# Optimization experiments

Measured on AMD Instinct MI355X. Metric: run time of the kernel, lower is better.

## Reference

```python
import jax, jax.numpy as jnp
import numpy as np

N, E, F, H, C = 100000, 1600000, 128, 128, 16
NEG_SLOPE = 0.01  # torch F.leaky_relu default


def setup_inputs() -> dict:
    key = jax.random.key(0)
    ks = jax.random.split(key, 32)
    inp = {
        "x": jax.random.normal(ks[0], (N, F), jnp.float32),
        "edge_index": jax.random.randint(ks[1], (2, E), 0, N, jnp.int32),
        "edge_weight": jax.random.uniform(ks[2], (E,), jnp.float32),
    }
    def w(k, fan_in, fan_out):
        s = 1.0 / np.sqrt(fan_in)
        return jax.random.uniform(k, (fan_in, fan_out), jnp.float32, -s, s)
    # cell 0: pre 128->128, arma 128->128, sage 128->128
    inp["pre_w0"] = w(ks[3], F, H); inp["pre_b0"] = jnp.zeros((H,), jnp.float32)
    inp["arma_w0"] = w(ks[4], H, H); inp["arma_v0"] = w(ks[5], H, H); inp["arma_b0"] = jnp.zeros((H,), jnp.float32)
    inp["sage_wl0"] = w(ks[6], H, H); inp["sage_bl0"] = jnp.zeros((H,), jnp.float32); inp["sage_wr0"] = w(ks[7], H, H)
    # cell 1: pre 256->128 (cell0 outputs 2H)
    inp["pre_w1"] = w(ks[8], 2 * H, H); inp["pre_b1"] = jnp.zeros((H,), jnp.float32)
    inp["arma_w1"] = w(ks[9], H, H); inp["arma_v1"] = w(ks[10], H, H); inp["arma_b1"] = jnp.zeros((H,), jnp.float32)
    inp["sage_wl1"] = w(ks[11], H, H); inp["sage_bl1"] = jnp.zeros((H,), jnp.float32); inp["sage_wr1"] = w(ks[12], H, H)
    inp["cls_w"] = w(ks[13], 2 * H, C); inp["cls_b"] = jnp.zeros((C,), jnp.float32)
    return inp


def _cell(h, row, col, norm, ew, cnt, n, arma_w, arma_v, arma_b, sage_wl, sage_bl, sage_wr):
    # ARMAConv (num_stacks=1, num_layers=1): relu(A_hat (h W) + h V + b), A_hat = sym-norm adj (no self loops)
    t = h @ arma_w
    agg = jax.ops.segment_sum(norm[:, None] * t[row], col, num_segments=n)
    h1 = jax.nn.leaky_relu(jax.nn.relu(agg + h @ arma_v + arma_b), NEG_SLOPE)
    # SAGEConv (mean aggr of edge-weighted messages): lin_l(mean_j w_ij h_j) + lin_r(h_i)
    s = jax.ops.segment_sum(ew[:, None] * h[row], col, num_segments=n)
    h2 = jax.nn.leaky_relu((s / cnt[:, None]) @ sage_wl + sage_bl + h @ sage_wr, NEG_SLOPE)
    return jax.nn.elu(jnp.concatenate([h1, h2], axis=1))


def reference(x, edge_index, edge_weight,
              pre_w0, pre_b0, arma_w0, arma_v0, arma_b0, sage_wl0, sage_bl0, sage_wr0,
              pre_w1, pre_b1, arma_w1, arma_v1, arma_b1, sage_wl1, sage_bl1, sage_wr1,
              cls_w, cls_b):
    n = x.shape[0]
    row, col = edge_index[0], edge_index[1]  # messages flow row -> col
    # gcn_norm without self loops (ARMAConv)
    deg = jax.ops.segment_sum(edge_weight, col, num_segments=n)
    dinv = jnp.where(deg > 0, 1.0 / jnp.sqrt(jnp.where(deg > 0, deg, 1.0)), 0.0)
    norm = dinv[row] * edge_weight * dinv[col]
    # scatter_mean denominator (edge counts, clamped to 1)
    cnt = jnp.maximum(jax.ops.segment_sum(jnp.ones_like(edge_weight), col, num_segments=n), 1.0)
    h = x  # eval mode: input dropout is identity
    for p in [(pre_w0, pre_b0, arma_w0, arma_v0, arma_b0, sage_wl0, sage_bl0, sage_wr0),
              (pre_w1, pre_b1, arma_w1, arma_v1, arma_b1, sage_wl1, sage_bl1, sage_wr1)]:
        pw, pb = p[0], p[1]
        h = _cell(h @ pw + pb, row, col, norm, edge_weight, cnt, n, *p[2:])
    logits = h @ cls_w + cls_b
    return jax.nn.log_softmax(logits, axis=-1)
```

## Files before the change

### kernel.cpp

```cpp
#include <hip/hip_runtime.h>
#include <hip/hip_bf16.h>
#include <hip/hip_fp16.h>

typedef __bf16 bf16x8 __attribute__((ext_vector_type(8)));
typedef float f32x4 __attribute__((ext_vector_type(4)));
typedef unsigned short ushort_t;
typedef unsigned int uint_t;

#if defined(__has_builtin)
#if __has_builtin(__builtin_amdgcn_global_load_lds)
#define HAS_GLL 1
#endif
#endif

__device__ inline float blo(uint_t v) { return __uint_as_float(v << 16); }
__device__ inline float bhi(uint_t v) { return __uint_as_float(v & 0xffff0000u); }
__device__ inline ushort_t f2b(float f) {
  uint_t u = __float_as_uint(f);
  uint_t r = (u + 0x7fffu + ((u >> 16) & 1u)) >> 16;
  return (ushort_t)r;
}
__device__ inline uint_t pk2(float a, float b) {
  return (uint_t)f2b(a) | ((uint_t)f2b(b) << 16);
}


__global__ __launch_bounds__(256) void bcount_k(const int* __restrict__ col,
                                                int* __restrict__ bcnt, int E, int NB) {
  __shared__ int h[256];
  int t = threadIdx.x;
  h[t] = 0;
  __syncthreads();
  int e0 = blockIdx.x * 8192;
#pragma unroll
  for (int j = 0; j < 32; ++j) {
    int e = e0 + j * 256 + t;
    if (e < E) atomicAdd(&h[col[e] >> 9], 1);
  }
  __syncthreads();
  if (t < NB && h[t] > 0) atomicAdd(&bcnt[t], h[t]);
}

__global__ __launch_bounds__(256) void bscan_k(const int* __restrict__ bcnt,
                                               int* __restrict__ bbase, int* __restrict__ cursor,
                                               int* __restrict__ offs, int NB, int N, int E) {
  __shared__ int sd[256];
  int t = threadIdx.x;
  int v = (t < NB) ? bcnt[t] : 0;
  int acc = v;
  sd[t] = v; __syncthreads();
  for (int off = 1; off < 256; off <<= 1) {
    int x = (t >= off) ? sd[t - off] : 0;
    __syncthreads();
    acc += x; sd[t] = acc;
    __syncthreads();
  }
  if (t < NB) { bbase[t] = acc - v; cursor[t] = acc - v; }
  if (t == 0) { bbase[NB] = E; offs[N] = E; }
}

__global__ __launch_bounds__(512) void bscatter_k(
    const int* __restrict__ row, const int* __restrict__ col, const float* __restrict__ ew,
    int* __restrict__ cursor, uint2* __restrict__ eout, int E, int NB) {
  __shared__ int h[256];
  __shared__ int lofs[256];
  __shared__ int lcur[256];
  __shared__ int gbase[256];
  __shared__ int sc[256];
  __shared__ uint2 stage[8192];
  __shared__ int addr[8192];
  int t = threadIdx.x;
  int e0 = blockIdx.x * 8192;
  int cnt = min(8192, E - e0);
  if (t < 256) h[t] = 0;
  __syncthreads();
#pragma unroll
  for (int j = 0; j < 16; ++j) {
    int e = e0 + j * 512 + t;
    if (e < E) atomicAdd(&h[col[e] >> 9], 1);
  }
  __syncthreads();
  int s = (t < 256) ? h[t] : 0;
  int acc = s;
  if (t < 256) sc[t] = s;
  __syncthreads();
  for (int off = 1; off < 256; off <<= 1) {
    int x = (t < 256 && t >= off) ? sc[t - off] : 0;
    __syncthreads();
    if (t < 256) { acc += x; sc[t] = acc; }
    __syncthreads();
  }
  if (t < NB && s > 0) gbase[t] = atomicAdd(&cursor[t], s);
  if (t < 256) { lofs[t] = acc - s; lcur[t] = acc - s; }
  __syncthreads();
#pragma unroll
  for (int j = 0; j < 16; ++j) {
    int e = e0 + j * 512 + t;
    if (e < E) {
      int c = col[e];
      int bk = c >> 9;
      int p = atomicAdd(&lcur[bk], 1);
      uint2 v;
      v.x = ((uint_t)(c & 511) << 17) | (uint_t)row[e];
      v.y = __float_as_uint(ew[e]);
      stage[p] = v;
      addr[p] = gbase[bk] + (p - lofs[bk]);
    }
  }
  __syncthreads();
  for (int i = t; i < cnt; i += 512) eout[addr[i]] = stage[i];
}

__global__ __launch_bounds__(512) void bsort_k(
    const uint2* __restrict__ ein, const int* __restrict__ bbase,
    int* __restrict__ offs, float* __restrict__ dinv, float* __restrict__ cinv,
    uint2* __restrict__ eout, int N) {
  __shared__ int h[512];
  __shared__ int lcur[512];
  __shared__ float degs[512];
  __shared__ int sd[512];
  int t = threadIdx.x, b = blockIdx.x;
  int base = bbase[b], end = bbase[b + 1];
  int cnt = end - base;
  int node0 = b << 9;
  h[t] = 0;
  degs[t] = 0.f;
  __syncthreads();
  for (int i = t; i < cnt; i += 512) {
    uint2 v = ein[base + i];
    int lc = v.x >> 17;
    atomicAdd(&h[lc], 1);
    atomicAdd(&degs[lc], __uint_as_float(v.y));
  }
  __syncthreads();
  int s = h[t];
  int acc = s;
  sd[t] = s; __syncthreads();
  for (int off = 1; off < 512; off <<= 1) {
    int x = (t >= off) ? sd[t - off] : 0;
    __syncthreads();
    acc += x; sd[t] = acc;
    __syncthreads();
  }
  int excl = acc - s;
  lcur[t] = excl;
  int node = node0 + t;
  if (node < N) {
    offs[node] = base + excl;
    float d = degs[t];
    dinv[node] = d > 0.f ? rsqrtf(d) : 0.f;
    cinv[node] = 1.0f / fmaxf((float)s, 1.f);
  }
  __syncthreads();
  for (int i = t; i < cnt; i += 512) {
    uint2 v = ein[base + i];
    int lc = v.x >> 17;
    int p = atomicAdd(&lcur[lc], 1);
    uint2 o;
    o.x = v.x & 0x1FFFF;
    o.y = v.y;
    eout[base + p] = o;
  }
}

__global__ void edgew_k(uint2* __restrict__ sedge, const float* __restrict__ dinv, int E) {
  int e = blockIdx.x * blockDim.x + threadIdx.x;
  if (e < E) {
    uint2 v = sedge[e];
    float ew = __uint_as_float(v.y);
    float wA = dinv[v.x] * ew;
    uint_t lo = (uint_t)__half_as_ushort(__float2half_rn(wA));
    uint_t hi = (uint_t)__half_as_ushort(__float2half_rn(ew));
    sedge[e].y = lo | (hi << 16);
  }
}

struct WP { const float* p[12]; };
__global__ void wtp_k(WP wp, ushort_t* __restrict__ wt) {
  int b = blockIdx.x;
  int t = threadIdx.x;
  if (b < 11) {
    const float* W = wp.p[b];
    ushort_t* T = wt + (size_t)b * 128 * 128;
    for (int i = 0; i < 64; ++i) {
      int lin = i * 256 + t;
      int k = lin >> 7, c = lin & 127;
      T[c * 128 + k] = f2b(W[lin]);
    }
  } else {
    const float* W = wp.p[11];
    ushort_t* T = wt + (size_t)11 * 128 * 128;
    for (int i = 0; i < 16; ++i) {
      int lin = i * 256 + t;
      int c = lin >> 8, k = lin & 255;
      T[lin] = f2b(W[k * 16 + c]);
    }
  }
}

__global__ __launch_bounds__(256) void agg_k(
    const uint_t* __restrict__ hp2, const uint2* __restrict__ sedge,
    const float* __restrict__ dinv, const float* __restrict__ cinv,
    const int* __restrict__ offs,
    uint_t* __restrict__ outA, uint_t* __restrict__ outS, int n) {
  int wid = threadIdx.x >> 6;
  int lane = threadIdx.x & 63;
  int half = lane >> 5, li = lane & 31;
  int node = blockIdx.x * 4 + wid;
  if (node >= n) return;
  int s0 = __builtin_amdgcn_readfirstlane(offs[node]);
  int e0 = __builtin_amdgcn_readfirstlane(offs[node + 1]);
  const char* hpb = (const char*)hp2;
  uint_t libase = (uint_t)(li << 3);
  float a0 = 0.f, a1 = 0.f, a2 = 0.f, a3 = 0.f;
  float m0 = 0.f, m1 = 0.f, m2 = 0.f, m3 = 0.f;
  for (int p = s0; p < e0; p += 8) {
    uint2 ed[4];
#pragma unroll
    for (int j = 0; j < 4; ++j) {
      int k = p + 2 * j + half;
      ed[j] = sedge[k < e0 ? k : s0];
    }
#pragma unroll
    for (int j = 0; j < 4; ++j) {
      int k = p + 2 * j + half;
      bool ok = (k < e0);
      uint_t w = ok ? ed[j].y : 0u;
      uint2 v = *(const uint2*)(hpb + ((ed[j].x << 8) | libase));
      float wA = __half2float(__ushort_as_half((ushort_t)(w & 0xffff)));
      float wS = __half2float(__ushort_as_half((ushort_t)(w >> 16)));
      float f0 = blo(v.x), f1 = bhi(v.x), f2 = blo(v.y), f3 = bhi(v.y);
      a0 += wA * f0; a1 += wA * f1; a2 += wA * f2; a3 += wA * f3;
      m0 += wS * f0; m1 += wS * f1; m2 += wS * f2; m3 += wS * f3;
    }
  }
  a0 += __shfl_xor(a0, 32); a1 += __shfl_xor(a1, 32);
  a2 += __shfl_xor(a2, 32); a3 += __shfl_xor(a3, 32);
  m0 += __shfl_xor(m0, 32); m1 += __shfl_xor(m1, 32);
  m2 += __shfl_xor(m2, 32); m3 += __shfl_xor(m3, 32);
  if (half == 0) {
    float dn = dinv[node];
    uint2 o;
    o.x = pk2(dn * a0, dn * a1);
    o.y = pk2(dn * a2, dn * a3);
    *(uint2*)&outA[(size_t)node * 64 + li * 2] = o;
  } else {
    float cn = cinv[node];
    uint2 o;
    o.x = pk2(cn * m0, cn * m1);
    o.y = pk2(cn * m2, cn * m3);
    *(uint2*)&outS[(size_t)node * 64 + li * 2] = o;
  }
}

__device__ inline int swz(int r, int k) { return (r * 128 + k) ^ ((r & 7) << 3); }
__device__ inline int cswz(int r, int k) { return (r * 256 + k) ^ ((r & 7) << 3); }

__device__ inline void stage_tile64(const ushort_t* __restrict__ A, ushort_t* lds,
                                    int rowBase, int wid, int lane) {
  int lr = lane >> 4, lchunk = lane & 15;
#ifdef HAS_GLL
#pragma unroll
  for (int i = 0; i < 4; ++i) {
    int r = wid * 16 + i * 4 + lr;
    int csrc = (lchunk ^ (r & 7)) << 4;
    const char* g = (const char*)A + (((size_t)(rowBase + r)) << 8) + csrc;
    char* l = (char*)lds + ((wid * 16 + i * 4) << 8);
    __builtin_amdgcn_global_load_lds((const __attribute__((address_space(1))) void*)g,
                                     (__attribute__((address_space(3))) void*)l, 16, 0, 0);
  }
#else
#pragma unroll
  for (int i = 0; i < 4; ++i) {
    int r = wid * 16 + i * 4 + lr;
    uint4 v = *(const uint4*)&A[((size_t)(rowBase + r)) * 128 + lchunk * 8];
    *(uint4*)&lds[swz(r, lchunk * 8)] = v;
  }
#endif
}

__device__ inline void stage_tile(const ushort_t* __restrict__ A, ushort_t* lds,
                                  int rowBase, int wid, int lane) {
  int lr = lane >> 4, lchunk = lane & 15;
#ifdef HAS_GLL
#pragma unroll
  for (int i = 0; i < 8; ++i) {
    int r = wid * 32 + i * 4 + lr;
    int csrc = (lchunk ^ (r & 7)) << 4;
    const char* g = (const char*)A + (((size_t)(rowBase + r)) << 8) + csrc;
    char* l = (char*)lds + ((wid * 32 + i * 4) << 8);
    __builtin_amdgcn_global_load_lds((const __attribute__((address_space(1))) void*)g,
                                     (__attribute__((address_space(3))) void*)l, 16, 0, 0);
  }
#else
#pragma unroll
  for (int i = 0; i < 8; ++i) {
    int r = wid * 32 + i * 4 + lr;
    uint4 v = *(const uint4*)&A[((size_t)(rowBase + r)) * 128 + lchunk * 8];
    *(uint4*)&lds[swz(r, lchunk * 8)] = v;
  }
#endif
}

__device__ inline void stage_wait() {
#ifdef HAS_GLL
  asm volatile("s_waitcnt vmcnt(0)" ::: "memory");
#endif
}

__device__ inline bf16x8 ldw(const ushort_t* __restrict__ Wt, int c, int k, int lane) {
  return *(const bf16x8*)&Wt[c * 128 + k * 32 + (lane >> 4) * 8];
}

__device__ inline bf16x8 lda64(const ushort_t* lds, int m, int k, int lane) {
  return *(const bf16x8*)&lds[swz(m * 16 + (lane & 15), k * 32 + (lane >> 4) * 8)];
}

__global__ __launch_bounds__(256, 2) void pre0_k(
    const float* __restrict__ Xf, const ushort_t* __restrict__ Wt,
    const float* __restrict__ bias, ushort_t* __restrict__ out, int nrows) {
  __shared__ ushort_t As[128 * 128];
  int t = threadIdx.x, lane = t & 63, wid = t >> 6;
  int wr = wid >> 1, wc = wid & 1;
  int rowBase = blockIdx.x * 128;
#pragma unroll
  for (int i = 0; i < 16; ++i) {
    int f = t + i * 256;
    int r = f >> 5, q = f & 31;
    int gr = rowBase + r;
    float4 v = make_float4(0.f, 0.f, 0.f, 0.f);
    if (gr < nrows) v = *(const float4*)&Xf[(size_t)gr * 128 + q * 4];
    uint2 o;
    o.x = pk2(v.x, v.y);
    o.y = pk2(v.z, v.w);
    *(uint2*)&As[swz(r, q * 4)] = o;
  }
  __syncthreads();
  f32x4 acc[4][4] = {};
#pragma unroll
  for (int k = 0; k < 4; ++k) {
    bf16x8 af[4], wf[4];
#pragma unroll
    for (int m = 0; m < 4; ++m)
      af[m] = *(const bf16x8*)&As[swz(wr * 64 + m * 16 + (lane & 15), k * 32 + (lane >> 4) * 8)];
#pragma unroll
    for (int nn = 0; nn < 4; ++nn) wf[nn] = ldw(Wt, wc * 64 + nn * 16 + (lane & 15), k, lane);
#pragma unroll
    for (int m = 0; m < 4; ++m)
#pragma unroll
      for (int nn = 0; nn < 4; ++nn)
        acc[m][nn] = __builtin_amdgcn_mfma_f32_16x16x32_bf16(af[m], wf[nn], acc[m][nn], 0, 0, 0);
  }
#pragma unroll
  for (int m = 0; m < 4; ++m) {
    int gr0 = rowBase + wr * 64 + m * 16 + (lane >> 4) * 4;
#pragma unroll
    for (int nn = 0; nn < 4; ++nn) {
      int gc = wc * 64 + nn * 16 + (lane & 15);
      float bv = bias[gc];
#pragma unroll
      for (int j = 0; j < 4; ++j) {
        int gr = gr0 + j;
        if (gr < nrows) out[(size_t)gr * 128 + gc] = f2b(acc[m][nn][j] + bv);
      }
    }
  }
}

template <int TAIL>
__global__ __launch_bounds__(256, 3) void dualfused_k(
    const ushort_t* __restrict__ X, const ushort_t* __restrict__ Y,
    const ushort_t* __restrict__ H,
    const ushort_t* __restrict__ WX, const ushort_t* __restrict__ WXH,
    const ushort_t* __restrict__ WY, const ushort_t* __restrict__ WYH,
    const float* __restrict__ bX, const float* __restrict__ bY,
    const ushort_t* __restrict__ WZ1, const ushort_t* __restrict__ WZ2,
    const float* __restrict__ bZ,
    ushort_t* __restrict__ outH, float* __restrict__ outL, int nrows) {
  __shared__ ushort_t buf[3 * 64 * 128];
  ushort_t* Xs = buf;
  ushort_t* Ys = buf + 64 * 128;
  ushort_t* Hs = buf + 2 * 64 * 128;
  int t = threadIdx.x, lane = t & 63, wid = t >> 6;
  int rowBase = blockIdx.x * 64;
  int c16 = lane & 15;

  stage_tile64(X, Xs, rowBase, wid, lane);
  stage_tile64(Y, Ys, rowBase, wid, lane);
  stage_tile64(H, Hs, rowBase, wid, lane);
  stage_wait();
  __syncthreads();

  f32x4 acc1[4][2] = {};
  f32x4 acc2[4][2] = {};
#pragma unroll
  for (int k = 0; k < 4; ++k) {
    bf16x8 xf[4], yf[4], hf[4], wx[2], whx[2], wy[2], why[2];
#pragma unroll
    for (int m = 0; m < 4; ++m) {
      xf[m] = lda64(Xs, m, k, lane);
      yf[m] = lda64(Ys, m, k, lane);
      hf[m] = lda64(Hs, m, k, lane);
    }
#pragma unroll
    for (int nn = 0; nn < 2; ++nn) {
      int c = wid * 32 + nn * 16 + c16;
      wx[nn] = ldw(WX, c, k, lane);
      whx[nn] = ldw(WXH, c, k, lane);
      wy[nn] = ldw(WY, c, k, lane);
      why[nn] = ldw(WYH, c, k, lane);
    }
#pragma unroll
    for (int m = 0; m < 4; ++m)
#pragma unroll
      for (int nn = 0; nn < 2; ++nn) {
        acc1[m][nn] = __builtin_amdgcn_mfma_f32_16x16x32_bf16(xf[m], wx[nn], acc1[m][nn], 0, 0, 0);
        acc1[m][nn] = __builtin_amdgcn_mfma_f32_16x16x32_bf16(hf[m], whx[nn], acc1[m][nn], 0, 0, 0);
        acc2[m][nn] = __builtin_amdgcn_mfma_f32_16x16x32_bf16(yf[m], wy[nn], acc2[m][nn], 0, 0, 0);
        acc2[m][nn] = __builtin_amdgcn_mfma_f32_16x16x32_bf16(hf[m], why[nn], acc2[m][nn], 0, 0, 0);
      }
  }

  __syncthreads();

#pragma unroll
  for (int m = 0; m < 4; ++m) {
    int r0 = m * 16 + (lane >> 4) * 4;
#pragma unroll
    for (int nn = 0; nn < 2; ++nn) {
      int c = wid * 32 + nn * 16 + c16;
      float bv1 = bX[c];
      float bv2 = bY[c];
#pragma unroll
      for (int j = 0; j < 4; ++j) {
        int r = r0 + j;
        float v1 = fmaxf(acc1[m][nn][j] + bv1, 0.f);
        buf[cswz(r, c)] = f2b(v1);
        float v2 = acc2[m][nn][j] + bv2;
        v2 = v2 > 0.f ? v2 : (__expf(0.01f * v2) - 1.f);
        buf[cswz(r, 128 + c)] = f2b(v2);
      }
    }
  }
  __syncthreads();

  if (TAIL == 0) {
    f32x4 acc3[4][2] = {};
#pragma unroll
    for (int kk = 0; kk < 8; ++kk) {
      const ushort_t* WZ = (kk < 4) ? WZ1 : WZ2;
      int kl = kk & 3;
      bf16x8 af[4], wf[2];
#pragma unroll
      for (int m = 0; m < 4; ++m)
        af[m] = *(const bf16x8*)&buf[cswz(m * 16 + c16, kk * 32 + (lane >> 4) * 8)];
#pragma unroll
      for (int nn = 0; nn < 2; ++nn) wf[nn] = ldw(WZ, wid * 32 + nn * 16 + c16, kl, lane);
#pragma unroll
      for (int m = 0; m < 4; ++m)
#pragma unroll
        for (int nn = 0; nn < 2; ++nn)
          acc3[m][nn] = __builtin_amdgcn_mfma_f32_16x16x32_bf16(af[m], wf[nn], acc3[m][nn], 0, 0, 0);
    }
#pragma unroll
    for (int m = 0; m < 4; ++m) {
      int gr0 = rowBase + m * 16 + (lane >> 4) * 4;
#pragma unroll
      for (int nn = 0; nn < 2; ++nn) {
        int gc = wid * 32 + nn * 16 + c16;
        float bv = bZ[gc];
#pragma unroll
        for (int j = 0; j < 4; ++j) {
          int gr = gr0 + j;
          if (gr < nrows) outH[(size_t)gr * 128 + gc] = f2b(acc3[m][nn][j] + bv);
        }
      }
    }
  } else {
    f32x4 accc = {};
#pragma unroll
    for (int kk = 0; kk < 8; ++kk) {
      bf16x8 bfr = *(const bf16x8*)&WZ1[c16 * 256 + kk * 32 + (lane >> 4) * 8];
      bf16x8 af = *(const bf16x8*)&buf[cswz(wid * 16 + c16, kk * 32 + (lane >> 4) * 8)];
      accc = __builtin_amdgcn_mfma_f32_16x16x32_bf16(af, bfr, accc, 0, 0, 0);
    }
    float bc = bZ[c16];
#pragma unroll
    for (int j = 0; j < 4; ++j) {
      float lg = accc[j] + bc;
      float mx = lg;
      for (int d = 1; d < 16; d <<= 1) mx = fmaxf(mx, __shfl_xor(mx, d));
      float ex = __expf(lg - mx);
      float sum = ex;
      for (int d = 1; d < 16; d <<= 1) sum += __shfl_xor(sum, d);
      float r_ = (lg - mx) - logf(sum);
      int grow = rowBase + wid * 16 + (lane >> 4) * 4 + j;
      if (grow < nrows) outL[grow * 16 + c16] = r_;
    }
  }
}


extern "C" void kernel_launch(void* const* d_in, const int* in_sizes, int n_in,
                              void* d_out, int out_size, void* d_ws, size_t ws_size,
                              hipStream_t stream) {
  const float* x        = (const float*)d_in[0];
  const int*   eidx     = (const int*)d_in[1];
  const float* ew       = (const float*)d_in[2];
  const float* pre_w0   = (const float*)d_in[3];
  const float* pre_b0   = (const float*)d_in[4];
  const float* arma_w0  = (const float*)d_in[5];
  const float* arma_v0  = (const float*)d_in[6];
  const float* arma_b0  = (const float*)d_in[7];
  const float* sage_wl0 = (const float*)d_in[8];
  const float* sage_bl0 = (const float*)d_in[9];
  const float* sage_wr0 = (const float*)d_in[10];
  const float* pre_w1   = (const float*)d_in[11];
  const float* pre_b1   = (const float*)d_in[12];
  const float* arma_w1  = (const float*)d_in[13];
  const float* arma_v1  = (const float*)d_in[14];
  const float* arma_b1  = (const float*)d_in[15];
  const float* sage_wl1 = (const float*)d_in[16];
  const float* sage_bl1 = (const float*)d_in[17];
  const float* sage_wr1 = (const float*)d_in[18];
  const float* cls_w    = (const float*)d_in[19];
  const float* cls_b    = (const float*)d_in[20];

  const int N = in_sizes[0] / 128;
  const int E = in_sizes[2];
  const int N_pad = ((N + 127) / 128) * 128;
  const int NB = (N + 511) >> 9;
  const int* row = eidx;
  const int* col = eidx + E;

  char* p = (char*)d_ws;
  auto carve = [&](size_t bytes) { char* q = p; p += (bytes + 255) & ~(size_t)255; return q; };
  ushort_t* hp    = (ushort_t*)carve((size_t)N_pad * 128 * 2);
  ushort_t* bufA  = (ushort_t*)carve((size_t)N_pad * 128 * 2);
  ushort_t* bufS  = (ushort_t*)carve((size_t)N_pad * 128 * 2);
  ushort_t* wt    = (ushort_t*)carve(((size_t)11 * 128 * 128 + 16 * 256) * 2);
  uint2*  sedge  = (uint2*)carve((size_t)E * 8);
  uint2*  sedgeT = (uint2*)carve((size_t)E * 8);
  float*  dinv  = (float*)carve((size_t)N * 4);
  float*  cinv  = (float*)carve((size_t)N * 4);
  int*    offs  = (int*)carve((size_t)(N + 1) * 4);
  int*    bcnt  = (int*)carve((size_t)256 * 4);
  int*    bbase = (int*)carve((size_t)257 * 4);
  int*    cursor= (int*)carve((size_t)256 * 4);

  hipMemsetAsync(bcnt, 0, (size_t)256 * 4, stream);

  const int gE = (E + 8191) / 8192;
  bcount_k<<<gE, 256, 0, stream>>>(col, bcnt, E, NB);
  bscan_k<<<1, 256, 0, stream>>>(bcnt, bbase, cursor, offs, NB, N, E);
  bscatter_k<<<gE, 512, 0, stream>>>(row, col, ew, cursor, sedgeT, E, NB);
  bsort_k<<<NB, 512, 0, stream>>>(sedgeT, bbase, offs, dinv, cinv, sedge, N);
  edgew_k<<<(E + 255) / 256, 256, 0, stream>>>(sedge, dinv, E);

  WP wp;
  wp.p[0] = pre_w0;  wp.p[1] = arma_w0; wp.p[2] = arma_v0;
  wp.p[3] = sage_wl0; wp.p[4] = sage_wr0;
  wp.p[5] = pre_w1;  wp.p[6] = pre_w1 + 128 * 128;
  wp.p[7] = arma_w1; wp.p[8] = arma_v1;
  wp.p[9] = sage_wl1; wp.p[10] = sage_wr1;
  wp.p[11] = cls_w;
  wtp_k<<<12, 256, 0, stream>>>(wp, wt);

  const int gB = (N + 127) / 128;
  const int gB64 = (N + 63) / 64;
  const int gA = (N + 3) / 4;
  auto WT = [&](int i) { return wt + (size_t)i * 128 * 128; };

  pre0_k<<<gB, 256, 0, stream>>>(x, WT(0), pre_b0, hp, N);
  agg_k<<<gA, 256, 0, stream>>>((const uint_t*)hp, sedge, dinv, cinv, offs,
                                (uint_t*)bufA, (uint_t*)bufS, N);
  dualfused_k<0><<<gB64, 256, 0, stream>>>(bufA, bufS, hp, WT(1), WT(2), WT(3), WT(4),
                                           arma_b0, sage_bl0, WT(5), WT(6), pre_b1,
                                           hp, nullptr, N);
  agg_k<<<gA, 256, 0, stream>>>((const uint_t*)hp, sedge, dinv, cinv, offs,
                                (uint_t*)bufA, (uint_t*)bufS, N);
  dualfused_k<1><<<gB64, 256, 0, stream>>>(bufA, bufS, hp, WT(7), WT(8), WT(9), WT(10),
                                           arma_b1, sage_bl1, WT(11), nullptr, cls_b,
                                           nullptr, (float*)d_out, N);
}
```

Baseline: 366.1 us.

## Merge bucket count with first pre-GEMM, unroll agg loop, coalesce epilogue stores

Folds the edge bucket-count kernel and the first pre-projection GEMM into one launch that dispatches on block index, so the two independent jobs share a grid and one kernel launch goes away. The GEMM epilogues in the prolog and dualfused kernels now stage bf16 results in LDS and write them back as 16-byte row-contiguous stores instead of scattered 2-byte writes. The aggregation loop is unrolled to 16 edges per iteration to keep more gathers in flight. The costs are an extra LDS round-trip and sync in the epilogues, and higher register pressure in the aggregation kernel.

```diff
diff --git a/kernel.cpp b/kernel.cpp
--- a/kernel.cpp
+++ b/kernel.cpp
@@ -24,22 +24,110 @@
   return (uint_t)f2b(a) | ((uint_t)f2b(b) << 16);
 }
 
-
-__global__ __launch_bounds__(256) void bcount_k(const int* __restrict__ col,
-                                                int* __restrict__ bcnt, int E, int NB) {
-  __shared__ int h[256];
+__device__ inline int swz(int r, int k) { return (r * 128 + k) ^ ((r & 7) << 3); }
+__device__ inline int cswz(int r, int k) { return (r * 256 + k) ^ ((r & 7) << 3); }
+
+__device__ inline bf16x8 ldw(const ushort_t* __restrict__ Wt, int c, int k, int lane) {
+  return *(const bf16x8*)&Wt[c * 128 + k * 32 + (lane >> 4) * 8];
+}
+
+struct WP { const float* p[12]; };
+__global__ void wtp_k(WP wp, ushort_t* __restrict__ wt) {
+  int b = blockIdx.x;
   int t = threadIdx.x;
-  h[t] = 0;
-  __syncthreads();
-  int e0 = blockIdx.x * 8192;
-#pragma unroll
-  for (int j = 0; j < 32; ++j) {
-    int e = e0 + j * 256 + t;
-    if (e < E) atomicAdd(&h[col[e] >> 9], 1);
-  }
-  __syncthreads();
-  if (t < NB && h[t] > 0) atomicAdd(&bcnt[t], h[t]);
-}
+  if (b < 11) {
+    const float* W = wp.p[b];
+    ushort_t* T = wt + (size_t)b * 128 * 128;
+    for (int i = 0; i < 64; ++i) {
+      int lin = i * 256 + t;
+      int k = lin >> 7, c = lin & 127;
+      T[c * 128 + k] = f2b(W[lin]);
+    }
+  } else {
+    const float* W = wp.p[11];
+    ushort_t* T = wt + (size_t)11 * 128 * 128;
+    for (int i = 0; i < 16; ++i) {
+      int lin = i * 256 + t;
+      int c = lin >> 8, k = lin & 255;
+      T[lin] = f2b(W[k * 16 + c]);
+    }
+  }
+}
+
+__global__ __launch_bounds__(256, 2) void prolog_k(
+    const int* __restrict__ col, int* __restrict__ bcnt, int E, int NB, int gE,
+    const float* __restrict__ Xf, const ushort_t* __restrict__ Wt0,
+    const float* __restrict__ bias0, ushort_t* __restrict__ outp, int nrows) {
+  __shared__ ushort_t As[128 * 128];
+  int b = blockIdx.x;
+  int t = threadIdx.x;
+  if (b < gE) {
+    int* h = (int*)As;
+    h[t] = 0;
+    __syncthreads();
+    int e0 = b * 8192;
+#pragma unroll
+    for (int j = 0; j < 32; ++j) {
+      int e = e0 + j * 256 + t;
+      if (e < E) atomicAdd(&h[col[e] >> 9], 1);
+    }
+    __syncthreads();
+    if (t < NB && h[t] > 0) atomicAdd(&bcnt[t], h[t]);
+    return;
+  }
+  int lane = t & 63, wid = t >> 6;
+  int wr = wid >> 1, wc = wid & 1;
+  int rowBase = (b - gE) * 128;
+#pragma unroll
+  for (int i = 0; i < 16; ++i) {
+    int f = t + i * 256;
+    int r = f >> 5, q = f & 31;
+    int gr = rowBase + r;
+    float4 v = make_float4(0.f, 0.f, 0.f, 0.f);
+    if (gr < nrows) v = *(const float4*)&Xf[(size_t)gr * 128 + q * 4];
+    uint2 o;
+    o.x = pk2(v.x, v.y);
+    o.y = pk2(v.z, v.w);
+    *(uint2*)&As[swz(r, q * 4)] = o;
+  }
+  __syncthreads();
+  f32x4 acc[4][4] = {};
+#pragma unroll
+  for (int k = 0; k < 4; ++k) {
+    bf16x8 af[4], wf[4];
+#pragma unroll
+    for (int m = 0; m < 4; ++m)
+      af[m] = *(const bf16x8*)&As[swz(wr * 64 + m * 16 + (lane & 15), k * 32 + (lane >> 4) * 8)];
+#pragma unroll
+    for (int nn = 0; nn < 4; ++nn) wf[nn] = ldw(Wt0, wc * 64 + nn * 16 + (lane & 15), k, lane);
+#pragma unroll
+    for (int m = 0; m < 4; ++m)
+#pragma unroll
+      for (int nn = 0; nn < 4; ++nn)
+        acc[m][nn] = __builtin_amdgcn_mfma_f32_16x16x32_bf16(af[m], wf[nn], acc[m][nn], 0, 0, 0);
+  }
+  __syncthreads();
+#pragma unroll
+  for (int m = 0; m < 4; ++m) {
+    int r0 = wr * 64 + m * 16 + (lane >> 4) * 4;
+#pragma unroll
+    for (int nn = 0; nn < 4; ++nn) {
+      int c = wc * 64 + nn * 16 + (lane & 15);
+      float bv = bias0[c];
+#pragma unroll
+      for (int j = 0; j < 4; ++j) As[(r0 + j) * 128 + c] = f2b(acc[m][nn][j] + bv);
+    }
+  }
+  __syncthreads();
+#pragma unroll
+  for (int i = 0; i < 8; ++i) {
+    int idx = t + i * 256;
+    int r = idx >> 4, q = idx & 15;
+    int gr = rowBase + r;
+    if (gr < nrows) *(uint4*)&outp[(size_t)gr * 128 + q * 8] = *(const uint4*)&As[r * 128 + q * 8];
+  }
+}
+
 
 __global__ __launch_bounds__(256) void bscan_k(const int* __restrict__ bcnt,
                                                int* __restrict__ bbase, int* __restrict__ cursor,
@@ -172,29 +260,6 @@
     uint_t lo = (uint_t)__half_as_ushort(__float2half_rn(wA));
     uint_t hi = (uint_t)__half_as_ushort(__float2half_rn(ew));
     sedge[e].y = lo | (hi << 16);
-  }
-}
-
-struct WP { const float* p[12]; };
-__global__ void wtp_k(WP wp, ushort_t* __restrict__ wt) {
-  int b = blockIdx.x;
-  int t = threadIdx.x;
-  if (b < 11) {
-    const float* W = wp.p[b];
-    ushort_t* T = wt + (size_t)b * 128 * 128;
-    for (int i = 0; i < 64; ++i) {
-      int lin = i * 256 + t;
-      int k = lin >> 7, c = lin & 127;
-      T[c * 128 + k] = f2b(W[lin]);
-    }
-  } else {
-    const float* W = wp.p[11];
-    ushort_t* T = wt + (size_t)11 * 128 * 128;
-    for (int i = 0; i < 16; ++i) {
-      int lin = i * 256 + t;
-      int c = lin >> 8, k = lin & 255;
-      T[lin] = f2b(W[k * 16 + c]);
-    }
   }
 }
 
@@ -214,15 +279,15 @@
   uint_t libase = (uint_t)(li << 3);
   float a0 = 0.f, a1 = 0.f, a2 = 0.f, a3 = 0.f;
   float m0 = 0.f, m1 = 0.f, m2 = 0.f, m3 = 0.f;
-  for (int p = s0; p < e0; p += 8) {
-    uint2 ed[4];
-#pragma unroll
-    for (int j = 0; j < 4; ++j) {
+  for (int p = s0; p < e0; p += 16) {
+    uint2 ed[8];
+#pragma unroll
+    for (int j = 0; j < 8; ++j) {
       int k = p + 2 * j + half;
       ed[j] = sedge[k < e0 ? k : s0];
     }
 #pragma unroll
-    for (int j = 0; j < 4; ++j) {
+    for (int j = 0; j < 8; ++j) {
       int k = p + 2 * j + half;
       bool ok = (k < e0);
       uint_t w = ok ? ed[j].y : 0u;
@@ -253,9 +318,6 @@
   }
 }
 
-__device__ inline int swz(int r, int k) { return (r * 128 + k) ^ ((r & 7) << 3); }
-__device__ inline int cswz(int r, int k) { return (r * 256 + k) ^ ((r & 7) << 3); }
-
 __device__ inline void stage_tile64(const ushort_t* __restrict__ A, ushort_t* lds,
                                     int rowBase, int wid, int lane) {
   int lr = lane >> 4, lchunk = lane & 15;
@@ -279,92 +341,14 @@
 #endif
 }
 
-__device__ inline void stage_tile(const ushort_t* __restrict__ A, ushort_t* lds,
-                                  int rowBase, int wid, int lane) {
-  int lr = lane >> 4, lchunk = lane & 15;
-#ifdef HAS_GLL
-#pragma unroll
-  for (int i = 0; i < 8; ++i) {
-    int r = wid * 32 + i * 4 + lr;
-    int csrc = (lchunk ^ (r & 7)) << 4;
-    const char* g = (const char*)A + (((size_t)(rowBase + r)) << 8) + csrc;
-    char* l = (char*)lds + ((wid * 32 + i * 4) << 8);
-    __builtin_amdgcn_global_load_lds((const __attribute__((address_space(1))) void*)g,
-                                     (__attribute__((address_space(3))) void*)l, 16, 0, 0);
-  }
-#else
-#pragma unroll
-  for (int i = 0; i < 8; ++i) {
-    int r = wid * 32 + i * 4 + lr;
-    uint4 v = *(const uint4*)&A[((size_t)(rowBase + r)) * 128 + lchunk * 8];
-    *(uint4*)&lds[swz(r, lchunk * 8)] = v;
-  }
-#endif
-}
-
 __device__ inline void stage_wait() {
 #ifdef HAS_GLL
   asm volatile("s_waitcnt vmcnt(0)" ::: "memory");
 #endif
 }
 
-__device__ inline bf16x8 ldw(const ushort_t* __restrict__ Wt, int c, int k, int lane) {
-  return *(const bf16x8*)&Wt[c * 128 + k * 32 + (lane >> 4) * 8];
-}
-
 __device__ inline bf16x8 lda64(const ushort_t* lds, int m, int k, int lane) {
   return *(const bf16x8*)&lds[swz(m * 16 + (lane & 15), k * 32 + (lane >> 4) * 8)];
-}
-
-__global__ __launch_bounds__(256, 2) void pre0_k(
-    const float* __restrict__ Xf, const ushort_t* __restrict__ Wt,
-    const float* __restrict__ bias, ushort_t* __restrict__ out, int nrows) {
-  __shared__ ushort_t As[128 * 128];
-  int t = threadIdx.x, lane = t & 63, wid = t >> 6;
-  int wr = wid >> 1, wc = wid & 1;
-  int rowBase = blockIdx.x * 128;
-#pragma unroll
-  for (int i = 0; i < 16; ++i) {
-    int f = t + i * 256;
-    int r = f >> 5, q = f & 31;
-    int gr = rowBase + r;
-    float4 v = make_float4(0.f, 0.f, 0.f, 0.f);
-    if (gr < nrows) v = *(const float4*)&Xf[(size_t)gr * 128 + q * 4];
-    uint2 o;
-    o.x = pk2(v.x, v.y);
-    o.y = pk2(v.z, v.w);
-    *(uint2*)&As[swz(r, q * 4)] = o;
-  }
-  __syncthreads();
-  f32x4 acc[4][4] = {};
-#pragma unroll
-  for (int k = 0; k < 4; ++k) {
-    bf16x8 af[4], wf[4];
-#pragma unroll
-    for (int m = 0; m < 4; ++m)
-      af[m] = *(const bf16x8*)&As[swz(wr * 64 + m * 16 + (lane & 15), k * 32 + (lane >> 4) * 8)];
-#pragma unroll
-    for (int nn = 0; nn < 4; ++nn) wf[nn] = ldw(Wt, wc * 64 + nn * 16 + (lane & 15), k, lane);
-#pragma unroll
-    for (int m = 0; m < 4; ++m)
-#pragma unroll
-      for (int nn = 0; nn < 4; ++nn)
-        acc[m][nn] = __builtin_amdgcn_mfma_f32_16x16x32_bf16(af[m], wf[nn], acc[m][nn], 0, 0, 0);
-  }
-#pragma unroll
-  for (int m = 0; m < 4; ++m) {
-    int gr0 = rowBase + wr * 64 + m * 16 + (lane >> 4) * 4;
-#pragma unroll
-    for (int nn = 0; nn < 4; ++nn) {
-      int gc = wc * 64 + nn * 16 + (lane & 15);
-      float bv = bias[gc];
-#pragma unroll
-      for (int j = 0; j < 4; ++j) {
-        int gr = gr0 + j;
-        if (gr < nrows) out[(size_t)gr * 128 + gc] = f2b(acc[m][nn][j] + bv);
-      }
-    }
-  }
 }
 
 template <int TAIL>
@@ -462,19 +446,25 @@
         for (int nn = 0; nn < 2; ++nn)
           acc3[m][nn] = __builtin_amdgcn_mfma_f32_16x16x32_bf16(af[m], wf[nn], acc3[m][nn], 0, 0, 0);
     }
+    ushort_t* Ob = Hs;
 #pragma unroll
     for (int m = 0; m < 4; ++m) {
-      int gr0 = rowBase + m * 16 + (lane >> 4) * 4;
+      int r0 = m * 16 + (lane >> 4) * 4;
 #pragma unroll
       for (int nn = 0; nn < 2; ++nn) {
-        int gc = wid * 32 + nn * 16 + c16;
-        float bv = bZ[gc];
-#pragma unroll
-        for (int j = 0; j < 4; ++j) {
-          int gr = gr0 + j;
-          if (gr < nrows) outH[(size_t)gr * 128 + gc] = f2b(acc3[m][nn][j] + bv);
-        }
+        int c = wid * 32 + nn * 16 + c16;
+        float bv = bZ[c];
+#pragma unroll
+        for (int j = 0; j < 4; ++j) Ob[(r0 + j) * 128 + c] = f2b(acc3[m][nn][j] + bv);
       }
+    }
+    __syncthreads();
+#pragma unroll
+    for (int i = 0; i < 4; ++i) {
+      int idx = t + i * 256;
+      int r = idx >> 4, q = idx & 15;
+      int gr = rowBase + r;
+      if (gr < nrows) *(uint4*)&outH[(size_t)gr * 128 + q * 8] = *(const uint4*)&Ob[r * 128 + q * 8];
     }
   } else {
     f32x4 accc = {};
@@ -551,11 +541,10 @@
   hipMemsetAsync(bcnt, 0, (size_t)256 * 4, stream);
 
   const int gE = (E + 8191) / 8192;
-  bcount_k<<<gE, 256, 0, stream>>>(col, bcnt, E, NB);
-  bscan_k<<<1, 256, 0, stream>>>(bcnt, bbase, cursor, offs, NB, N, E);
-  bscatter_k<<<gE, 512, 0, stream>>>(row, col, ew, cursor, sedgeT, E, NB);
-  bsort_k<<<NB, 512, 0, stream>>>(sedgeT, bbase, offs, dinv, cinv, sedge, N);
-  edgew_k<<<(E + 255) / 256, 256, 0, stream>>>(sedge, dinv, E);
+  const int gB = (N + 127) / 128;
+  const int gB64 = (N + 63) / 64;
+  const int gA = (N + 3) / 4;
+  auto WT = [&](int i) { return wt + (size_t)i * 128 * 128; };
 
   WP wp;
   wp.p[0] = pre_w0;  wp.p[1] = arma_w0; wp.p[2] = arma_v0;
@@ -564,14 +553,14 @@
   wp.p[7] = arma_w1; wp.p[8] = arma_v1;
   wp.p[9] = sage_wl1; wp.p[10] = sage_wr1;
   wp.p[11] = cls_w;
+
   wtp_k<<<12, 256, 0, stream>>>(wp, wt);
-
-  const int gB = (N + 127) / 128;
-  const int gB64 = (N + 63) / 64;
-  const int gA = (N + 3) / 4;
-  auto WT = [&](int i) { return wt + (size_t)i * 128 * 128; };
-
-  pre0_k<<<gB, 256, 0, stream>>>(x, WT(0), pre_b0, hp, N);
+  prolog_k<<<gE + gB, 256, 0, stream>>>(col, bcnt, E, NB, gE, x, WT(0), pre_b0, hp, N);
+  bscan_k<<<1, 256, 0, stream>>>(bcnt, bbase, cursor, offs, NB, N, E);
+  bscatter_k<<<gE, 512, 0, stream>>>(row, col, ew, cursor, sedgeT, E, NB);
+  bsort_k<<<NB, 512, 0, stream>>>(sedgeT, bbase, offs, dinv, cinv, sedge, N);
+  edgew_k<<<(E + 255) / 256, 256, 0, stream>>>(sedge, dinv, E);
+
   agg_k<<<gA, 256, 0, stream>>>((const uint_t*)hp, sedge, dinv, cinv, offs,
                                 (uint_t*)bufA, (uint_t*)bufS, N);
   dualfused_k<0><<<gB64, 256, 0, stream>>>(bufA, bufS, hp, WT(1), WT(2), WT(3), WT(4),
```

New measurement: 369.2 us. About the same (+0.8%).
